# Kernel tuning notes

Measured on AMD Instinct MI355X. Metric: run time of the kernel, lower is better.

## Reference

```python
import jax, jax.numpy as jnp
import numpy as np

B, S, H, NH, NL = 8, 768, 768, 12, 5
HD = H // NH


def setup_inputs() -> dict:
    key = jax.random.key(0)
    ks = jax.random.split(key, 14)
    lim = 1.0 / np.sqrt(H)
    u = lambda k, shape: jax.random.uniform(k, shape, jnp.float32, -lim, lim)
    inp = {}
    inp["hidden_states"] = jax.random.normal(ks[0], (B, S, H), jnp.float32)
    inp["language_ids"] = jax.random.randint(ks[1], (B,), 0, NL)
    inp["attention_mask"] = jnp.ones((B, S), jnp.int32)
    # per-language query/key Linear weights (torch Linear: y = x @ W.T + b)
    inp["Wq_lang"] = u(ks[2], (NL, H, H))
    inp["bq_lang"] = u(ks[3], (NL, H))
    inp["Wk_lang"] = u(ks[4], (NL, H, H))
    inp["bk_lang"] = u(ks[5], (NL, H))
    # nn.MultiheadAttention params
    inp["in_proj_w"] = u(ks[6], (3 * H, H))
    inp["in_proj_b"] = u(ks[7], (3 * H,))
    inp["out_proj_w"] = u(ks[8], (H, H))
    inp["out_proj_b"] = u(ks[9], (H,))
    # alignment matrices: initialized as eye in torch; perturb so products are non-trivial
    inp["align"] = jnp.eye(H, dtype=jnp.float32) + 0.02 * jax.random.normal(ks[10], (NL, NL, H, H), jnp.float32)
    # output projection + layer norm
    inp["proj_w"] = u(ks[11], (H, H))
    inp["proj_b"] = u(ks[12], (H,))
    inp["ln_g"] = jnp.ones((H,), jnp.float32)
    inp["ln_b"] = jnp.zeros((H,), jnp.float32)
    return inp


def reference(hidden_states, language_ids, attention_mask, Wq_lang, bq_lang, Wk_lang, bk_lang,
              in_proj_w, in_proj_b, out_proj_w, out_proj_b, align, proj_w, proj_b, ln_g, ln_b):
    b, s, h = hidden_states.shape
    lang = language_ids
    # language-routed query/key transforms (grouped GEMM via gather of per-lang weights)
    q = jnp.einsum('bsi,boi->bso', hidden_states, Wq_lang[lang]) + bq_lang[lang][:, None, :]
    k = jnp.einsum('bsi,boi->bso', hidden_states, Wk_lang[lang]) + bk_lang[lang][:, None, :]
    # nn.MultiheadAttention (eval mode, no dropout). Note: the torch module's
    # key_padding_mask is always all-False due to a masked_fill(-inf).bool() bug,
    # so no masking is applied -- reproduced faithfully here.
    wq, wk, wv = jnp.split(in_proj_w, 3, axis=0)
    bq_, bk_, bv_ = jnp.split(in_proj_b, 3)
    Q = (jnp.einsum('bsi,oi->bso', q, wq) + bq_).reshape(b, s, NH, HD)
    K = (jnp.einsum('bsi,oi->bso', k, wk) + bk_).reshape(b, s, NH, HD)
    V = (jnp.einsum('bsi,oi->bso', hidden_states, wv) + bv_).reshape(b, s, NH, HD)
    scores = jnp.einsum('bqhd,bkhd->bhqk', Q, K) / np.sqrt(HD).astype(np.float32)
    attn = jax.nn.softmax(scores, axis=-1)  # [b, nh, s, s]
    ctx = jnp.einsum('bhqk,bkhd->bqhd', attn, V).reshape(b, s, h)
    aligned = jnp.einsum('bsi,oi->bso', ctx, out_proj_w) + out_proj_b
    # pairwise alignment chain: for each i, aligned_i @ prod_{j: lang_j != lang_i} A[lang_i, lang_j]
    # (i==j skipped; same-language pairs skipped since no A exists)
    same = lang[:, None] == lang[None, :]  # [b, b]; diagonal is True -> identity
    sel = align[lang[:, None], lang[None, :]]  # [b, b, h, h]
    I = jnp.eye(h, dtype=hidden_states.dtype)
    Smat = jnp.where(same[:, :, None, None], I, sel)  # [b(i), b(j), h, h]
    def step(carry, Sj):  # carry [b,h,h], Sj [b,h,h] for one j across all i
        return carry @ Sj, None
    M, _ = jax.lax.scan(step, jnp.tile(I, (b, 1, 1)), jnp.swapaxes(Smat, 0, 1))
    aligned = jnp.einsum('bsh,bhk->bsk', aligned, M)
    # output projection + residual layer norm
    out = jnp.einsum('bsi,oi->bso', aligned, proj_w) + proj_b
    x = out + hidden_states
    mu = x.mean(-1, keepdims=True)
    var = x.var(-1, keepdims=True)
    return (x - mu) / jnp.sqrt(var + 1e-5) * ln_g + ln_b
```

## Files before the change

### kernel.cpp

```cpp
#include <hip/hip_runtime.h>

#define Bn 8
#define Sn 768
#define Hn 768
#define NHn 12
#define HDn 64
#define NLn 5

typedef unsigned short u16;
typedef __bf16 bf16x8 __attribute__((ext_vector_type(8)));
typedef short s16x8 __attribute__((ext_vector_type(8)));
typedef float f32x4 __attribute__((ext_vector_type(4)));
typedef unsigned short u16x4 __attribute__((ext_vector_type(4)));

static __device__ __forceinline__ float bf2f(u16 v) {
    return __uint_as_float(((unsigned)v) << 16);
}
static __device__ __forceinline__ u16 f2bf(float f) {
    unsigned u = __float_as_uint(f);
    unsigned r = u + 0x7fffu + ((u >> 16) & 1u);
    return (u16)(r >> 16);
}
static __device__ __forceinline__ bf16x8 ld8(const u16* p) {
    return *reinterpret_cast<const bf16x8*>(p);
}
static __device__ __forceinline__ void glds16(const u16* g, u16* l) {
    __builtin_amdgcn_global_load_lds(
        (const __attribute__((address_space(1))) void*)g,
        (__attribute__((address_space(3))) void*)l, 16, 0, 0);
}

#define PREP_NF2B 6912
#define PREP_NTR  1584
__global__ __launch_bounds__(256) void k_prep(
    const float* __restrict__ hidden, u16* __restrict__ hb,
    const float* __restrict__ ipw, u16* __restrict__ ipwb,
    const float* __restrict__ projw, u16* __restrict__ pjwb,
    const float* __restrict__ Wq, const float* __restrict__ Wk,
    const float* __restrict__ opw, u16* __restrict__ S, u16* __restrict__ opwT,
    const float* __restrict__ ipb,
    const float* __restrict__ bq_lang, const float* __restrict__ bk_lang,
    float* __restrict__ beff)
{
    __shared__ float T[64][65];
    const size_t HH = (size_t)Hn * Hn;
    const int bid = blockIdx.x, tid = threadIdx.x;
    if (bid < PREP_NF2B) {
        const int n0 = (int)(Bn * Sn * Hn / 4), n1 = (int)(3 * HH / 4), n2 = (int)(HH / 4);
        int i = bid * 256 + tid;
        const float* s; u16* d; int off;
        if (i < n0)                { s = hidden; d = hb;   off = i; }
        else if (i < n0 + n1)      { s = ipw;    d = ipwb; off = i - n0; }
        else if (i < n0 + n1 + n2) { s = projw;  d = pjwb; off = i - n0 - n1; }
        else return;
        float4 v = reinterpret_cast<const float4*>(s)[off];
        u16x4 o;
        o[0] = f2bf(v.x); o[1] = f2bf(v.y); o[2] = f2bf(v.z); o[3] = f2bf(v.w);
        reinterpret_cast<u16x4*>(d)[off] = o;
    } else if (bid < PREP_NF2B + PREP_NTR) {
        int b2 = bid - PREP_NF2B;
        int z = b2 / 144, r = b2 % 144;
        int bx = r % 12, by = r / 12;
        const float* src;
        u16* dst;
        if (z < 5)       { src = Wq + (size_t)z * HH;       dst = S + (size_t)z * HH; }
        else if (z < 10) { src = Wk + (size_t)(z - 5) * HH; dst = S + (size_t)z * HH; }
        else             { src = opw;                        dst = opwT; }
        int i0 = bx * 64, o0 = by * 64;
        int x = tid & 63, ys = tid >> 6;
        for (int rr = ys; rr < 64; rr += 4)
            T[rr][x] = src[(size_t)(o0 + rr) * Hn + i0 + x];
        __syncthreads();
        for (int rr = ys; rr < 64; rr += 4)
            dst[(size_t)(i0 + rr) * Hn + o0 + x] = f2bf(T[x][rr]);
    } else {
        int b3 = bid - PREP_NF2B - PREP_NTR;
        int ox = b3 % 3, y = b3 / 3;
        int o = ox * 256 + tid;
        int which = y / 5, l = y % 5;
        const float4* w = reinterpret_cast<const float4*>(ipw + (size_t)which * HH + (size_t)o * Hn);
        const float4* bv = reinterpret_cast<const float4*>(((which ? bk_lang : bq_lang) + (size_t)l * Hn));
        float s = 0.f;
        for (int j = 0; j < Hn / 4; ++j) {
            float4 a = w[j], b = bv[j];
            s += a.x * b.x + a.y * b.y + a.z * b.z + a.w * b.w;
        }
        s += ipb[which * Hn + o];
        beff[(size_t)(which * 5 + l) * Hn + o] = s;
    }
}

__global__ __launch_bounds__(256) void k_f2b1(
    const float* __restrict__ s, u16* __restrict__ d, int n)
{
    int i = blockIdx.x * 256 + threadIdx.x;
    if (i >= n) return;
    float4 v = reinterpret_cast<const float4*>(s)[i];
    u16x4 o;
    o[0] = f2bf(v.x); o[1] = f2bf(v.y); o[2] = f2bf(v.z); o[3] = f2bf(v.w);
    reinterpret_cast<u16x4*>(d)[i] = o;
}

template<int TM>
__device__ __forceinline__ void gemm_core(
    const u16* __restrict__ A, int lda,
    const u16* __restrict__ Bw, int ldb,
    const float* __restrict__ bias,
    const float* __restrict__ addres,
    u16* __restrict__ outH, float* __restrict__ outF,
    u16* __restrict__ outVT, int ldc,
    int m0, int n0, float scale)
{
    constexpr int MI = TM / 32;
    constexpr int AIT = TM / 64;
    __shared__ u16 As[3 * TM * 32];
    __shared__ u16 Bs[3 * 128 * 32];
    const int tid = threadIdx.x;
    const int lane = tid & 63, wave = tid >> 6;
    const int lrow = lane & 15, lquad = lane >> 4;
    const int wm = (wave >> 1) * (TM / 2), wn = (wave & 1) * 64;

    const u16* gA = A + (size_t)(m0 + (tid >> 2)) * lda + (tid & 3) * 8;
    const u16* gB = Bw + (size_t)(n0 + (tid >> 2)) * ldb + (tid & 3) * 8;

    f32x4 z = {0.f, 0.f, 0.f, 0.f};
    f32x4 acc[MI][4];
    #pragma unroll
    for (int i = 0; i < MI; ++i)
        #pragma unroll
        for (int j = 0; j < 4; ++j) acc[i][j] = z;

    auto stage = [&](int bs, int k0) {
        #pragma unroll
        for (int it = 0; it < AIT; ++it)
            glds16(gA + (size_t)(it * 64) * lda + k0, &As[bs * TM * 32 + (tid + 256 * it) * 8]);
        #pragma unroll
        for (int it = 0; it < 2; ++it)
            glds16(gB + (size_t)(it * 64) * ldb + k0, &Bs[bs * 128 * 32 + (tid + 256 * it) * 8]);
    };
    auto compute = [&](int bc) {
        const u16* Ab = &As[bc * TM * 32];
        const u16* Bb = &Bs[bc * 128 * 32];
        bf16x8 af[MI], bf_[4];
        #pragma unroll
        for (int i = 0; i < MI; ++i)
            af[i] = ld8(&Ab[(wm + i * 16 + lrow) * 32 + lquad * 8]);
        #pragma unroll
        for (int j = 0; j < 4; ++j)
            bf_[j] = ld8(&Bb[(wn + j * 16 + lrow) * 32 + lquad * 8]);
        #pragma unroll
        for (int i = 0; i < MI; ++i)
            #pragma unroll
            for (int j = 0; j < 4; ++j)
                acc[i][j] = __builtin_amdgcn_mfma_f32_16x16x32_bf16(af[i], bf_[j], acc[i][j], 0, 0, 0);
    };

    stage(0, 0);
    stage(1, 32);
    int bc = 0, bs = 2;
    for (int kt = 0; kt < 24; ++kt) {
        if (kt < 23) {
            if constexpr (TM == 256) {
                asm volatile("s_waitcnt vmcnt(6)" ::: "memory");
            } else {
                asm volatile("s_waitcnt vmcnt(4)" ::: "memory");
            }
        } else {
            asm volatile("s_waitcnt vmcnt(0)" ::: "memory");
        }
        __builtin_amdgcn_s_barrier();
        if (kt < 22) {
            stage(bs, (kt + 2) * 32);
            bs = (bs == 2) ? 0 : bs + 1;
        }
        compute(bc);
        bc = (bc == 2) ? 0 : bc + 1;
    }

    #pragma unroll
    for (int i = 0; i < MI; ++i) {
        #pragma unroll
        for (int j = 0; j < 4; ++j) {
            int col = n0 + wn + j * 16 + lrow;
            float bv = bias ? bias[col] : 0.f;
            if (outVT) {
                int row0 = m0 + wm + i * 16 + lquad * 4;
                int bb = row0 / Sn, s = row0 % Sn;
                int hh = col >> 6, dd = col & 63;
                u16x4 o;
                #pragma unroll
                for (int r = 0; r < 4; ++r) o[r] = f2bf((acc[i][j][r] + bv) * scale);
                *reinterpret_cast<u16x4*>(
                    outVT + (((size_t)bb * NHn + hh) * 64 + dd) * Sn + s) = o;
            } else {
                #pragma unroll
                for (int r = 0; r < 4; ++r) {
                    int row = m0 + wm + i * 16 + lquad * 4 + r;
                    float v = (acc[i][j][r] + bv) * scale;
                    if (addres) v += addres[(size_t)row * ldc + col];
                    if (outF) outF[(size_t)row * ldc + col] = v;
                    else      outH[(size_t)row * ldc + col] = f2bf(v);
                }
            }
        }
    }
}

__device__ __forceinline__ void gemm64(
    const u16* __restrict__ A, const u16* __restrict__ Bw,
    u16* __restrict__ outH, int m0, int n0)
{
    __shared__ u16 As[3 * 64 * 32];
    __shared__ u16 Bs[3 * 64 * 32];
    const int tid = threadIdx.x;
    const int lane = tid & 63, wave = tid >> 6;
    const int lrow = lane & 15, lquad = lane >> 4;
    const int wm = (wave >> 1) * 32, wn = (wave & 1) * 32;

    const u16* gA = A + (size_t)(m0 + (tid >> 2)) * Hn + (tid & 3) * 8;
    const u16* gB = Bw + (size_t)(n0 + (tid >> 2)) * Hn + (tid & 3) * 8;

    f32x4 z = {0.f, 0.f, 0.f, 0.f};
    f32x4 acc[2][2];
    #pragma unroll
    for (int i = 0; i < 2; ++i)
        #pragma unroll
        for (int j = 0; j < 2; ++j) acc[i][j] = z;

    auto stage = [&](int bs, int k0) {
        glds16(gA + k0, &As[bs * 64 * 32 + tid * 8]);
        glds16(gB + k0, &Bs[bs * 64 * 32 + tid * 8]);
    };
    auto compute = [&](int bc) {
        const u16* Ab = &As[bc * 64 * 32];
        const u16* Bb = &Bs[bc * 64 * 32];
        bf16x8 af[2], bf_[2];
        #pragma unroll
        for (int i = 0; i < 2; ++i)
            af[i] = ld8(&Ab[(wm + i * 16 + lrow) * 32 + lquad * 8]);
        #pragma unroll
        for (int j = 0; j < 2; ++j)
            bf_[j] = ld8(&Bb[(wn + j * 16 + lrow) * 32 + lquad * 8]);
        #pragma unroll
        for (int i = 0; i < 2; ++i)
            #pragma unroll
            for (int j = 0; j < 2; ++j)
                acc[i][j] = __builtin_amdgcn_mfma_f32_16x16x32_bf16(af[i], bf_[j], acc[i][j], 0, 0, 0);
    };

    stage(0, 0);
    stage(1, 32);
    int bc = 0, bs = 2;
    for (int kt = 0; kt < 24; ++kt) {
        if (kt < 23) {
            asm volatile("s_waitcnt vmcnt(2)" ::: "memory");
        } else {
            asm volatile("s_waitcnt vmcnt(0)" ::: "memory");
        }
        __builtin_amdgcn_s_barrier();
        if (kt < 22) {
            stage(bs, (kt + 2) * 32);
            bs = (bs == 2) ? 0 : bs + 1;
        }
        compute(bc);
        bc = (bc == 2) ? 0 : bc + 1;
    }

    #pragma unroll
    for (int i = 0; i < 2; ++i)
        #pragma unroll
        for (int j = 0; j < 2; ++j) {
            int col = n0 + wn + j * 16 + lrow;
            #pragma unroll
            for (int r = 0; r < 4; ++r) {
                int row_ = m0 + wm + i * 16 + lquad * 4 + r;
                outH[(size_t)row_ * Hn + col] = f2bf(acc[i][j][r]);
            }
        }
}


__global__ __launch_bounds__(256, 2) void k_gemm_qkv(
    const u16* __restrict__ A,
    const u16* __restrict__ Sq, const u16* __restrict__ Sk,
    const u16* __restrict__ Wv,
    const float* __restrict__ beff, const float* __restrict__ ipb,
    const int* __restrict__ lang,
    u16* __restrict__ outQ, u16* __restrict__ outK, u16* __restrict__ outVT)
{
    const size_t HH = (size_t)Hn * Hn;
    int z = blockIdx.z;
    int m0 = blockIdx.x * 256, n0 = blockIdx.y * 128;
    int l = lang[blockIdx.x / 3];
    if (z == 0) {
        gemm_core<256>(A, Hn, Sq + (size_t)l * HH, Hn, beff + (size_t)l * Hn,
                       nullptr, outQ, nullptr, nullptr, Hn, m0, n0, 0.125f);
    } else if (z == 1) {
        gemm_core<256>(A, Hn, Sk + (size_t)l * HH, Hn, beff + (size_t)(5 + l) * Hn,
                       nullptr, outK, nullptr, nullptr, Hn, m0, n0, 1.f);
    } else {
        gemm_core<256>(A, Hn, Wv, Hn, ipb + 2 * Hn,
                       nullptr, nullptr, nullptr, outVT, Hn, m0, n0, 1.f);
    }
}

__global__ __launch_bounds__(256) void k_comb10(
    const u16* __restrict__ ipwb, u16* __restrict__ S)
{
    const size_t HH = (size_t)Hn * Hn;
    int z = blockIdx.z;
    const u16* Aop = ipwb + (z < 5 ? 0 : HH);
    gemm_core<128>(Aop, Hn, S + (size_t)z * HH, Hn, nullptr, nullptr,
                   S + (size_t)(10 + z) * HH, nullptr, nullptr, Hn,
                   blockIdx.x * 128, blockIdx.y * 128, 1.f);
}

__global__ __launch_bounds__(256) void k_chain_first(
    const u16* __restrict__ alignb, const int* __restrict__ lang,
    u16* __restrict__ out5)
{
    const size_t HH = (size_t)Hn * Hn;
    int l = blockIdx.z, lj = lang[Bn - 1];
    u16* dst = out5 + (size_t)l * HH;
    int i0 = blockIdx.x * 64, o0 = blockIdx.y * 64;
    const int tid = threadIdx.x;
    if (lj == l) {
        #pragma unroll
        for (int it = 0; it < 2; ++it) {
            int s = tid + 256 * it;
            int ri = s >> 3, c8 = s & 7;
            s16x8 v;
            #pragma unroll
            for (int e = 0; e < 8; ++e)
                v[e] = (short)((i0 + ri == o0 + c8 * 8 + e) ? 0x3F80 : 0);
            *reinterpret_cast<s16x8*>(dst + (size_t)(i0 + ri) * Hn + o0 + c8 * 8) = v;
        }
    } else {
        const u16* src = alignb + ((size_t)l * NLn + lj) * HH;
        __shared__ u16 T[64][72];
        #pragma unroll
        for (int it = 0; it < 2; ++it) {
            int s = tid + 256 * it;
            int r = s >> 3, c8 = s & 7;
            s16x8 v = *reinterpret_cast<const s16x8*>(
                src + (size_t)(o0 + r) * Hn + i0 + c8 * 8);
            #pragma unroll
            for (int e = 0; e < 8; ++e) T[c8 * 8 + e][r] = (u16)v[e];
        }
        __syncthreads();
        #pragma unroll
        for (int it = 0; it < 2; ++it) {
            int s = tid + 256 * it;
            int ri = s >> 3, c8 = s & 7;
            s16x8 v = *reinterpret_cast<const s16x8*>(&T[ri][c8 * 8]);
            *reinterpret_cast<s16x8*>(dst + (size_t)(i0 + ri) * Hn + o0 + c8 * 8) = v;
        }
    }
}

__global__ __launch_bounds__(256) void k_chain64(
    const u16* __restrict__ Pin, u16* __restrict__ Pout,
    const u16* __restrict__ alignb, const int* __restrict__ lang, int j)
{
    const size_t HH = (size_t)Hn * Hn;
    int l = blockIdx.z;
    int lj = lang[j];
    const u16* Pl = Pin + (size_t)l * HH;
    u16* Po = Pout + (size_t)l * HH;
    int m0 = blockIdx.x * 64, n0 = blockIdx.y * 64;
    if (lj == l) {
        int tid = threadIdx.x;
        #pragma unroll
        for (int it = 0; it < 2; ++it) {
            int s = tid + 256 * it;
            int row = s >> 3, seg = s & 7;
            *reinterpret_cast<s16x8*>(Po + (size_t)(m0 + row) * Hn + n0 + seg * 8) =
                *reinterpret_cast<const s16x8*>(Pl + (size_t)(m0 + row) * Hn + n0 + seg * 8);
        }
    } else {
        const u16* F = alignb + ((size_t)l * NLn + lj) * HH;
        gemm64(Pl, F, Po, m0, n0);
    }
}

__global__ __launch_bounds__(256) void k_uop(
    const u16* __restrict__ opwT, const u16* __restrict__ MT5,
    const float* __restrict__ opb,
    u16* __restrict__ U5, float* __restrict__ opbeff)
{
    const size_t HH = (size_t)Hn * Hn;
    int bid = blockIdx.x;
    if (bid < 720) {
        int z = bid / 144, r = bid % 144;
        gemm64(opwT, MT5 + (size_t)z * HH, U5 + (size_t)z * HH,
               (r % 12) * 64, (r / 12) * 64);
    } else {
        int b2 = bid - 720;
        int n = (b2 % 3) * 256 + threadIdx.x;
        int l = b2 / 3;
        const u16* mt = MT5 + ((size_t)l * Hn + n) * Hn;
        float s = 0.f;
        for (int k = 0; k < Hn; k += 8) {
            s16x8 v = *reinterpret_cast<const s16x8*>(mt + k);
            #pragma unroll
            for (int j = 0; j < 8; ++j) s += opb[k + j] * bf2f((u16)v[j]);
        }
        opbeff[(size_t)l * Hn + n] = s;
    }
}

__global__ __launch_bounds__(256) void k_wb2(
    const u16* __restrict__ pjwb, const u16* __restrict__ U5,
    const float* __restrict__ opbeff, const float* __restrict__ projw,
    const float* __restrict__ projb,
    u16* __restrict__ W5, float* __restrict__ bias2)
{
    const size_t HH = (size_t)Hn * Hn;
    int bid = blockIdx.x;
    if (bid < 720) {
        int z = bid / 144, r = bid % 144;
        gemm64(pjwb, U5 + (size_t)z * HH, W5 + (size_t)z * HH,
               (r % 12) * 64, (r / 12) * 64);
    } else {
        int b2 = bid - 720;
        int m = (b2 % 3) * 256 + threadIdx.x;
        int l = b2 / 3;
        const float4* w = reinterpret_cast<const float4*>(projw + (size_t)m * Hn);
        const float4* ob = reinterpret_cast<const float4*>(opbeff + (size_t)l * Hn);
        float s = 0.f;
        for (int j = 0; j < Hn / 4; ++j) {
            float4 a = w[j], b = ob[j];
            s += a.x * b.x + a.y * b.y + a.z * b.z + a.w * b.w;
        }
        bias2[(size_t)l * Hn + m] = s + projb[m];
    }
}

__global__ __launch_bounds__(256) void k_xfused(
    const u16* __restrict__ ctx, const u16* __restrict__ W5,
    const float* __restrict__ bias2, const int* __restrict__ lang,
    const float* __restrict__ hidden, float* __restrict__ x)
{
    int l = lang[blockIdx.x / 6];
    gemm_core<128>(ctx, Hn, W5 + (size_t)l * Hn * Hn, Hn, bias2 + (size_t)l * Hn,
                   hidden, nullptr, x, nullptr, Hn,
                   blockIdx.x * 128, blockIdx.y * 128, 1.f);
}

__global__ __launch_bounds__(512) void k_attn(
    const u16* __restrict__ Q, const u16* __restrict__ K,
    const u16* __restrict__ VT, u16* __restrict__ ctx)
{
    __shared__ u16 Ks[2][64 * 64];
    __shared__ u16 Vs[64 * 64];
    __shared__ u16 Pw[8][16 * 72];

    const int bz = blockIdx.z, h = blockIdx.y, q0 = blockIdx.x * 128;
    const int tid = threadIdx.x;
    const int wave = tid >> 6, lane = tid & 63;
    const int lrow = lane & 15, lquad = lane >> 4;
    const int sw = lrow & 7;

    const u16* Qp = Q + ((size_t)(bz * Sn + q0 + wave * 16 + lrow)) * Hn + h * HDn;
    const u16* Kb = K + (size_t)bz * Sn * Hn + h * HDn;
    const u16* Vb = VT + ((size_t)(bz * NHn + h) * 64) * Sn;

    bf16x8 qa0 = ld8(Qp + lquad * 8);
    bf16x8 qa1 = ld8(Qp + 32 + lquad * 8);

    f32x4 z4 = {0.f, 0.f, 0.f, 0.f};
    float m_r[4], l_l[4];
    f32x4 oacc[4];
    #pragma unroll
    for (int r = 0; r < 4; ++r) { m_r[r] = -1e30f; l_l[r] = 0.f; }
    #pragma unroll
    for (int jd = 0; jd < 4; ++jd) oacc[jd] = z4;

    const int vd0 = tid >> 3, vp0 = (tid & 7) ^ (vd0 & 7);
    const u16* vg0 = Vb + (size_t)vd0 * Sn + vp0 * 8;
    s16x8 vr0;

    auto vload = [&](int t0) {
        vr0 = *reinterpret_cast<const s16x8*>(vg0 + t0);
    };
    auto vstore = [&]() {
        *reinterpret_cast<s16x8*>(&Vs[tid * 8]) = vr0;
    };
    auto stageK = [&](int t0, int buf) {
        int row = tid >> 3, p = tid & 7;
        glds16(Kb + (size_t)(t0 + row) * Hn + (p ^ (row & 7)) * 8,
               &Ks[buf][tid * 8]);
    };

    auto compute = [&](int buf) {
        f32x4 sc[4];
        __builtin_amdgcn_s_setprio(1);
        #pragma unroll
        for (int j = 0; j < 4; ++j) {
            int base = (j * 16 + lrow) * 64 + ((lquad ^ sw) * 8);
            f32x4 s = __builtin_amdgcn_mfma_f32_16x16x32_bf16(qa0, ld8(&Ks[buf][base]), z4, 0, 0, 0);
            sc[j] = __builtin_amdgcn_mfma_f32_16x16x32_bf16(qa1, ld8(&Ks[buf][base ^ 32]), s, 0, 0, 0);
        }
        __builtin_amdgcn_s_setprio(0);
        float tmax[4];
        #pragma unroll
        for (int r = 0; r < 4; ++r)
            tmax[r] = fmaxf(fmaxf(sc[0][r], sc[1][r]), fmaxf(sc[2][r], sc[3][r]));
        #pragma unroll
        for (int off = 1; off < 16; off <<= 1)
            #pragma unroll
            for (int r = 0; r < 4; ++r)
                tmax[r] = fmaxf(tmax[r], __shfl_xor(tmax[r], off));
        bool grow = (tmax[0] > m_r[0]) | (tmax[1] > m_r[1]) |
                    (tmax[2] > m_r[2]) | (tmax[3] > m_r[3]);
        if (grow) {
            #pragma unroll
            for (int r = 0; r < 4; ++r) {
                float mn = fmaxf(m_r[r], tmax[r]);
                float a = __expf(m_r[r] - mn);
                m_r[r] = mn;
                l_l[r] *= a;
                #pragma unroll
                for (int jd = 0; jd < 4; ++jd) oacc[jd][r] *= a;
            }
        }
        float ps[4] = {0.f, 0.f, 0.f, 0.f};
        #pragma unroll
        for (int j = 0; j < 4; ++j)
            #pragma unroll
            for (int r = 0; r < 4; ++r) {
                float p = __expf(sc[j][r] - m_r[r]);
                ps[r] += p;
                Pw[wave][(lquad * 4 + r) * 72 + j * 16 + lrow] = f2bf(p);
            }
        #pragma unroll
        for (int r = 0; r < 4; ++r) l_l[r] += ps[r];
        bf16x8 pa0 = ld8(&Pw[wave][lrow * 72 + lquad * 8]);
        bf16x8 pa1 = ld8(&Pw[wave][lrow * 72 + 32 + lquad * 8]);
        __builtin_amdgcn_s_setprio(1);
        #pragma unroll
        for (int jd = 0; jd < 4; ++jd) {
            int vbase = (jd * 16 + lrow) * 64 + ((lquad ^ sw) * 8);
            oacc[jd] = __builtin_amdgcn_mfma_f32_16x16x32_bf16(pa0, ld8(&Vs[vbase]), oacc[jd], 0, 0, 0);
            oacc[jd] = __builtin_amdgcn_mfma_f32_16x16x32_bf16(pa1, ld8(&Vs[vbase ^ 32]), oacc[jd], 0, 0, 0);
        }
        __builtin_amdgcn_s_setprio(0);
    };

    stageK(0, 0);
    vload(0);
    vstore();
    __syncthreads();
    for (int kt = 0; kt < 12; ++kt) {
        if (kt < 11) {
            vload((kt + 1) * 64);
            stageK((kt + 1) * 64, (kt + 1) & 1);
        }
        compute(kt & 1);
        if (kt < 11) {
            __syncthreads();
            vstore();
            __syncthreads();
        }
    }

    #pragma unroll
    for (int off = 1; off < 16; off <<= 1)
        #pragma unroll
        for (int r = 0; r < 4; ++r)
            l_l[r] += __shfl_xor(l_l[r], off);

    float rl[4];
    #pragma unroll
    for (int r = 0; r < 4; ++r) rl[r] = 1.f / l_l[r];
    #pragma unroll
    for (int jd = 0; jd < 4; ++jd)
        #pragma unroll
        for (int r = 0; r < 4; ++r) {
            size_t row = (size_t)bz * Sn + q0 + wave * 16 + lquad * 4 + r;
            ctx[row * Hn + h * HDn + jd * 16 + lrow] = f2bf(oacc[jd][r] * rl[r]);
        }
}

__global__ __launch_bounds__(64) void k_ln(
    float* x, const float* __restrict__ g, const float* __restrict__ beta)
{
    size_t row = blockIdx.x;
    float* xr = x + row * Hn;
    int lane = threadIdx.x;
    float v[12];
    float s = 0.f, ss = 0.f;
    #pragma unroll
    for (int i = 0; i < 12; ++i) {
        v[i] = xr[lane + i * 64];
        s += v[i];
        ss += v[i] * v[i];
    }
    #pragma unroll
    for (int off = 1; off < 64; off <<= 1) {
        s  += __shfl_xor(s, off);
        ss += __shfl_xor(ss, off);
    }
    float mu = s * (1.f / Hn);
    float var = ss * (1.f / Hn) - mu * mu;
    float inv = rsqrtf(var + 1e-5f);
    #pragma unroll
    for (int i = 0; i < 12; ++i) {
        int c = lane + i * 64;
        xr[c] = (v[i] - mu) * inv * g[c] + beta[c];
    }
}

extern "C" void kernel_launch(void* const* d_in, const int* in_sizes, int n_in,
                              void* d_out, int out_size, void* d_ws, size_t ws_size,
                              hipStream_t stream)
{
    (void)in_sizes; (void)n_in; (void)out_size; (void)ws_size;

    const float* hidden  = (const float*)d_in[0];
    const int*   lang    = (const int*)d_in[1];
    const float* Wq_lang = (const float*)d_in[3];
    const float* bq_lang = (const float*)d_in[4];
    const float* Wk_lang = (const float*)d_in[5];
    const float* bk_lang = (const float*)d_in[6];
    const float* ipw     = (const float*)d_in[7];
    const float* ipb     = (const float*)d_in[8];
    const float* opw     = (const float*)d_in[9];
    const float* opb     = (const float*)d_in[10];
    const float* align   = (const float*)d_in[11];
    const float* projw   = (const float*)d_in[12];
    const float* projb   = (const float*)d_in[13];
    const float* ln_g    = (const float*)d_in[14];
    const float* ln_b    = (const float*)d_in[15];
    float* out = (float*)d_out;

    const size_t HH  = (size_t)Hn * Hn;
    const size_t BSH = (size_t)Bn * Sn * Hn;
    const size_t AHH = (size_t)NLn * NLn * HH;

    u16* rA = (u16*)d_ws;
    u16* rB = rA + BSH;
    u16* rC = rB + BSH;
    u16* rD = rC + BSH;
    u16* ipwb = rD + BSH;
    u16* pjwb = ipwb + 3 * HH;
    u16* opwT = pjwb + HH;
    u16* alignb = opwT + HH;
    float* beff   = (float*)(alignb + AHH);
    float* opbeff = beff + 10 * Hn;
    float* bias2  = opbeff + 5 * Hn;

    u16* S = alignb;

    k_prep<<<(unsigned)(PREP_NF2B + PREP_NTR + 30), 256, 0, stream>>>(
        hidden, rA, ipw, ipwb, projw, pjwb,
        Wq_lang, Wk_lang, opw, S, opwT,
        ipb, bq_lang, bk_lang, beff);

    k_comb10<<<dim3(6, 6, 10), 256, 0, stream>>>(ipwb, S);

    k_gemm_qkv<<<dim3(24, 6, 3), 256, 0, stream>>>(
        rA, S + 10 * HH, S + 15 * HH, ipwb + 2 * HH, beff, ipb, lang, rB, rC, rD);

    k_f2b1<<<(unsigned)(AHH / 4 / 256), 256, 0, stream>>>(align, alignb, (int)(AHH / 4));

    k_attn<<<dim3(6, NHn, Bn), 512, 0, stream>>>(rB, rC, rD, rA);

    k_chain_first<<<dim3(12, 12, NLn), 256, 0, stream>>>(alignb, lang, rC);
    u16* Pin = rC;
    u16* Pout = rD;
    for (int j = Bn - 2; j >= 0; --j) {
        k_chain64<<<dim3(12, 12, NLn), 256, 0, stream>>>(Pin, Pout, alignb, lang, j);
        u16* t = Pin; Pin = Pout; Pout = t;
    }

    k_uop<<<735, 256, 0, stream>>>(opwT, Pin, opb, rB, opbeff);
    k_wb2<<<735, 256, 0, stream>>>(pjwb, rB, opbeff, projw, projb, rC, bias2);

    k_xfused<<<dim3(48, 6), 256, 0, stream>>>(rA, rC, bias2, lang, hidden, out);
    k_ln<<<(unsigned)(Bn * Sn), 64, 0, stream>>>(out, ln_g, ln_b);
}
```

Before: 513.9 us.

## Triple-buffer K/V via direct-to-LDS loads and fuse align conversion into attention

The attention kernel now stages both K and V tiles with global-to-LDS loads into a three-deep ring buffer. Each iteration waits on the vmcnt counter and issues one barrier, where it previously went through registers with two barriers. The standalone fp32-to-bf16 conversion of the alignment tensor is folded into the same launch as extra trailing blocks, which removes one kernel launch. LDS use per block grows, which may cut occupancy, and the conversion blocks now run at 512 threads alongside the attention blocks.

Result: faster. 500.2 us (-2.7%).

```diff
diff --git a/kernel.cpp b/kernel.cpp
--- a/kernel.cpp
+++ b/kernel.cpp
@@ -90,17 +90,6 @@
     }
 }
 
-__global__ __launch_bounds__(256) void k_f2b1(
-    const float* __restrict__ s, u16* __restrict__ d, int n)
-{
-    int i = blockIdx.x * 256 + threadIdx.x;
-    if (i >= n) return;
-    float4 v = reinterpret_cast<const float4*>(s)[i];
-    u16x4 o;
-    o[0] = f2bf(v.x); o[1] = f2bf(v.y); o[2] = f2bf(v.z); o[3] = f2bf(v.w);
-    reinterpret_cast<u16x4*>(d)[i] = o;
-}
-
 template<int TM>
 __device__ __forceinline__ void gemm_core(
     const u16* __restrict__ A, int lda,
@@ -447,16 +436,26 @@
                    blockIdx.x * 128, blockIdx.y * 128, 1.f);
 }
 
-__global__ __launch_bounds__(512) void k_attn(
+__global__ __launch_bounds__(512) void k_attn_conv(
     const u16* __restrict__ Q, const u16* __restrict__ K,
-    const u16* __restrict__ VT, u16* __restrict__ ctx)
-{
-    __shared__ u16 Ks[2][64 * 64];
-    __shared__ u16 Vs[64 * 64];
+    const u16* __restrict__ VT, u16* __restrict__ ctx,
+    const float* __restrict__ alignf, u16* __restrict__ alignb)
+{
+    __shared__ u16 Ks[3][64 * 64];
+    __shared__ u16 Vs[3][64 * 64];
     __shared__ u16 Pw[8][16 * 72];
 
-    const int bz = blockIdx.z, h = blockIdx.y, q0 = blockIdx.x * 128;
-    const int tid = threadIdx.x;
+    const int bid = blockIdx.x, tid = threadIdx.x;
+    if (bid >= 576) {
+        int i = (bid - 576) * 512 + tid;
+        float4 v = reinterpret_cast<const float4*>(alignf)[i];
+        u16x4 o;
+        o[0] = f2bf(v.x); o[1] = f2bf(v.y); o[2] = f2bf(v.z); o[3] = f2bf(v.w);
+        reinterpret_cast<u16x4*>(alignb)[i] = o;
+        return;
+    }
+
+    const int q0 = (bid % 6) * 128, h = (bid / 6) % NHn, bz = bid / 72;
     const int wave = tid >> 6, lane = tid & 63;
     const int lrow = lane & 15, lquad = lane >> 4;
     const int sw = lrow & 7;
@@ -476,30 +475,23 @@
     #pragma unroll
     for (int jd = 0; jd < 4; ++jd) oacc[jd] = z4;
 
-    const int vd0 = tid >> 3, vp0 = (tid & 7) ^ (vd0 & 7);
-    const u16* vg0 = Vb + (size_t)vd0 * Sn + vp0 * 8;
-    s16x8 vr0;
-
-    auto vload = [&](int t0) {
-        vr0 = *reinterpret_cast<const s16x8*>(vg0 + t0);
+    const int krow = tid >> 3, kp = (tid & 7) ^ (krow & 7);
+    const u16* kg = Kb + (size_t)krow * Hn + kp * 8;
+    const u16* vg = Vb + (size_t)krow * Sn + kp * 8;
+
+    auto stage = [&](int bs, int t0) {
+        glds16(kg + (size_t)t0 * Hn, &Ks[bs][tid * 8]);
+        glds16(vg + t0, &Vs[bs][tid * 8]);
     };
-    auto vstore = [&]() {
-        *reinterpret_cast<s16x8*>(&Vs[tid * 8]) = vr0;
-    };
-    auto stageK = [&](int t0, int buf) {
-        int row = tid >> 3, p = tid & 7;
-        glds16(Kb + (size_t)(t0 + row) * Hn + (p ^ (row & 7)) * 8,
-               &Ks[buf][tid * 8]);
-    };
-
-    auto compute = [&](int buf) {
+
+    auto compute = [&](int bc) {
         f32x4 sc[4];
         __builtin_amdgcn_s_setprio(1);
         #pragma unroll
         for (int j = 0; j < 4; ++j) {
             int base = (j * 16 + lrow) * 64 + ((lquad ^ sw) * 8);
-            f32x4 s = __builtin_amdgcn_mfma_f32_16x16x32_bf16(qa0, ld8(&Ks[buf][base]), z4, 0, 0, 0);
-            sc[j] = __builtin_amdgcn_mfma_f32_16x16x32_bf16(qa1, ld8(&Ks[buf][base ^ 32]), s, 0, 0, 0);
+            f32x4 s = __builtin_amdgcn_mfma_f32_16x16x32_bf16(qa0, ld8(&Ks[bc][base]), z4, 0, 0, 0);
+            sc[j] = __builtin_amdgcn_mfma_f32_16x16x32_bf16(qa1, ld8(&Ks[bc][base ^ 32]), s, 0, 0, 0);
         }
         __builtin_amdgcn_s_setprio(0);
         float tmax[4];
@@ -541,27 +533,28 @@
         #pragma unroll
         for (int jd = 0; jd < 4; ++jd) {
             int vbase = (jd * 16 + lrow) * 64 + ((lquad ^ sw) * 8);
-            oacc[jd] = __builtin_amdgcn_mfma_f32_16x16x32_bf16(pa0, ld8(&Vs[vbase]), oacc[jd], 0, 0, 0);
-            oacc[jd] = __builtin_amdgcn_mfma_f32_16x16x32_bf16(pa1, ld8(&Vs[vbase ^ 32]), oacc[jd], 0, 0, 0);
+            oacc[jd] = __builtin_amdgcn_mfma_f32_16x16x32_bf16(pa0, ld8(&Vs[bc][vbase]), oacc[jd], 0, 0, 0);
+            oacc[jd] = __builtin_amdgcn_mfma_f32_16x16x32_bf16(pa1, ld8(&Vs[bc][vbase ^ 32]), oacc[jd], 0, 0, 0);
         }
         __builtin_amdgcn_s_setprio(0);
     };
 
-    stageK(0, 0);
-    vload(0);
-    vstore();
-    __syncthreads();
+    stage(0, 0);
+    stage(1, 64);
+    int bc = 0, bs = 2;
     for (int kt = 0; kt < 12; ++kt) {
         if (kt < 11) {
-            vload((kt + 1) * 64);
-            stageK((kt + 1) * 64, (kt + 1) & 1);
-        }
-        compute(kt & 1);
-        if (kt < 11) {
-            __syncthreads();
-            vstore();
-            __syncthreads();
-        }
+            asm volatile("s_waitcnt vmcnt(2)" ::: "memory");
+        } else {
+            asm volatile("s_waitcnt vmcnt(0)" ::: "memory");
+        }
+        __builtin_amdgcn_s_barrier();
+        if (kt < 10) {
+            stage(bs, (kt + 2) * 64);
+            bs = (bs == 2) ? 0 : bs + 1;
+        }
+        compute(bc);
+        bc = (bc == 2) ? 0 : bc + 1;
     }
 
     #pragma unroll
@@ -662,9 +655,7 @@
     k_gemm_qkv<<<dim3(24, 6, 3), 256, 0, stream>>>(
         rA, S + 10 * HH, S + 15 * HH, ipwb + 2 * HH, beff, ipb, lang, rB, rC, rD);
 
-    k_f2b1<<<(unsigned)(AHH / 4 / 256), 256, 0, stream>>>(align, alignb, (int)(AHH / 4));
-
-    k_attn<<<dim3(6, NHn, Bn), 512, 0, stream>>>(rB, rC, rD, rA);
+    k_attn_conv<<<7776, 512, 0, stream>>>(rB, rC, rD, rA, align, alignb);
 
     k_chain_first<<<dim3(12, 12, NLn), 256, 0, stream>>>(alignb, lang, rC);
     u16* Pin = rC;
```
